# Optimization experiments

Hardware: AMD Instinct MI355X
Metric: run time of the kernel (lower is better)

## Reference

```python
import jax, jax.numpy as jnp
import numpy as np

B, T, I, H = 512, 256, 256, 512


def _lstm(x, Wih, Whh, bih, bhh):
    # x: [B, T, I]; Wih: [4H, I]; Whh: [4H, H]; gate order i, f, g, o (torch)
    Bv = x.shape[0]
    Hv = Whh.shape[1]
    xg = jnp.einsum('bti,gi->btg', x, Wih) + bih + bhh  # [B, T, 4H] (input projections hoisted out of scan)
    xg = jnp.transpose(xg, (1, 0, 2))  # [T, B, 4H]
    h0 = jnp.zeros((Bv, Hv), x.dtype)
    c0 = jnp.zeros((Bv, Hv), x.dtype)

    def step(carry, gx):
        h, c = carry
        g = gx + h @ Whh.T  # [B, 4H]
        i, f, gg, o = jnp.split(g, 4, axis=-1)
        i = jax.nn.sigmoid(i)
        f = jax.nn.sigmoid(f)
        gg = jnp.tanh(gg)
        o = jax.nn.sigmoid(o)
        c = f * c + i * gg
        h = o * jnp.tanh(c)
        return (h, c), h

    _, hs = jax.lax.scan(step, (h0, c0), xg)  # hs: [T, B, H]
    return jnp.transpose(hs, (1, 0, 2))  # [B, T, H]


def _bn1d(x, gamma, beta, eps=1e-5):
    # torch BatchNorm1d on [N, C, L] in training mode: per-channel stats over (N, L), biased var
    m = jnp.mean(x, axis=(0, 2), keepdims=True)
    v = jnp.var(x, axis=(0, 2), keepdims=True)
    return (x - m) * jax.lax.rsqrt(v + eps) * gamma[None, :, None] + beta[None, :, None]


def setup_inputs() -> dict:
    key = jax.random.key(0)
    ks = jax.random.split(key, 14)
    s = 1.0 / np.sqrt(H)
    return {
        'x': jax.random.normal(ks[0], (B, T, I), jnp.float32),
        'Wih': jax.random.uniform(ks[1], (4 * H, I), jnp.float32, -s, s),
        'Whh': jax.random.uniform(ks[2], (4 * H, H), jnp.float32, -s, s),
        'bih': jax.random.uniform(ks[3], (4 * H,), jnp.float32, -s, s),
        'bhh': jax.random.uniform(ks[4], (4 * H,), jnp.float32, -s, s),
        'fc1_w': jax.random.uniform(ks[5], (32, H), jnp.float32, -s, s),
        'fc1_b': jax.random.uniform(ks[6], (32,), jnp.float32, -s, s),
        'fc2_w': jax.random.uniform(ks[7], (1, 32), jnp.float32, -0.17, 0.17),
        'fc2_b': jax.random.uniform(ks[8], (1,), jnp.float32, -0.17, 0.17),
        'bn1_g': jnp.ones((T,), jnp.float32),
        'bn1_b': jnp.zeros((T,), jnp.float32),
        'bn2_g': jnp.ones((T,), jnp.float32),
        'bn2_b': jnp.zeros((T,), jnp.float32),
    }


def reference(x, Wih, Whh, bih, bhh, fc1_w, fc1_b, fc2_w, fc2_b, bn1_g, bn1_b, bn2_g, bn2_b):
    lstm_out = _lstm(x, Wih, Whh, bih, bhh)  # [B, T, H]
    a = jnp.einsum('bth,oh->bto', lstm_out, fc1_w) + fc1_b  # [B, T, 32]
    a = jax.nn.leaky_relu(_bn1d(a, bn1_g, bn1_b), negative_slope=0.1)
    z = jnp.einsum('bto,po->btp', a, fc2_w) + fc2_b  # [B, T, 1]
    out = jax.nn.relu(_bn1d(z, bn2_g, bn2_b))
    return out
```

## Files before the change

kernel.cpp:

```cpp
#include <hip/hip_runtime.h>

#define BB 512
#define TT 256
#define II 256
#define HH 512

typedef __attribute__((ext_vector_type(8))) short bf16x8;
typedef __attribute__((ext_vector_type(4))) float f32x4;

__device__ __forceinline__ unsigned short f2bf(float f) {
  union { float f; unsigned u; } v; v.f = f;
  unsigned r = v.u + 0x7fffu + ((v.u >> 16) & 1u);
  return (unsigned short)(r >> 16);
}

#define OFF_CNT   0
#define OFF_HSWZ  4096
#define OFF_XSWZ  1052672ULL
#define OFF_HIST  68161536ULL
#define ZERO_WORDS 263168

__global__ void zero_k(unsigned* __restrict__ p, int n) {
  int i = blockIdx.x * blockDim.x + threadIdx.x;
  if (i < n) p[i] = 0u;
}

__global__ __launch_bounds__(256) void prep_x(const float* __restrict__ x,
                                              unsigned char* __restrict__ ws) {
  __shared__ unsigned short xs[16][264];
  const int t = blockIdx.x >> 5, rc = blockIdx.x & 31;
  const int tid = threadIdx.x;
  {
    const int r = tid >> 4, seg = tid & 15;
    const float* src = x + ((size_t)(rc * 16 + r) * TT + t) * II + seg * 16;
    const float4* s4 = (const float4*)src;
#pragma unroll
    for (int q = 0; q < 4; ++q) {
      float4 v = s4[q];
      xs[r][seg * 16 + q * 4 + 0] = f2bf(v.x);
      xs[r][seg * 16 + q * 4 + 1] = f2bf(v.y);
      xs[r][seg * 16 + q * 4 + 2] = f2bf(v.z);
      xs[r][seg * 16 + q * 4 + 3] = f2bf(v.w);
    }
  }
  __syncthreads();
  const int lane = tid & 63;
  const int row16 = lane & 15, koff = (lane >> 4) * 8;
#pragma unroll
  for (int kc = tid >> 6; kc < 8; kc += 4) {
    union { unsigned short h[8]; uint4 v; } pk;
#pragma unroll
    for (int j = 0; j < 8; ++j) pk.h[j] = xs[row16][kc * 32 + koff + j];
    *(uint4*)(ws + OFF_XSWZ + (size_t)(t * 8 + kc) * 32768u +
              ((size_t)rc * 64 + lane) * 16) = pk.v;
  }
}

__global__ __launch_bounds__(512, 2) void lstm_persist(
    const float* __restrict__ Wih, const float* __restrict__ Whh,
    const float* __restrict__ bih, const float* __restrict__ bhh,
    unsigned char* __restrict__ ws)
{
  const int gid = blockIdx.x;
  const int g = gid & 31;
  const int m = gid >> 5;
  const int tid = threadIdx.x;
  const int wv = tid >> 6, lane = tid & 63;
  const int nh = wv & 3, kh = wv >> 2;
  const int lq = lane >> 4, ln = lane & 15;

  int* flags_g = (int*)(ws + (size_t)g * 128);
  unsigned char* xswz  = ws + OFF_XSWZ;
  unsigned char* hswz0 = ws + OFF_HSWZ;
  unsigned char* hswz1 = ws + OFF_HSWZ + 524288;
  unsigned char* hist  = ws + OFF_HIST;

  __shared__ int step_flag;
  if (tid == 0) step_flag = 0;

  bf16x8 Wf[12][4];
#pragma unroll
  for (int kk = 0; kk < 12; ++kk) {
    const int kb = (kh * 12 + kk) * 32 + lq * 8;
#pragma unroll
    for (int ns = 0; ns < 4; ++ns) {
      const int gcol = nh * 512 + m * 64 + ns * 16 + ln;
      const float* s = (kb < 256) ? (Wih + (size_t)gcol * 256 + kb)
                                  : (Whh + (size_t)gcol * 512 + (kb - 256));
      bf16x8 w;
#pragma unroll
      for (int j = 0; j < 8; ++j) w[j] = (short)f2bf(s[j]);
      Wf[kk][ns] = w;
    }
  }

  const int urow = tid >> 5;
  const int ujl  = (tid & 31) * 2;
  float bia2[2][4];
#pragma unroll
  for (int cc = 0; cc < 2; ++cc)
#pragma unroll
    for (int nt = 0; nt < 4; ++nt) {
      int gcol = nt * 512 + m * 64 + ujl + cc;
      bia2[cc][nt] = bih[gcol] + bhh[gcol];
    }

  __shared__ float g_s[8704];
  __shared__ float h_s[1088];
  __shared__ unsigned long long hstage[2048];

  float c2[2] = {0.f, 0.f};
  const f32x4 zero4 = {0.f, 0.f, 0.f, 0.f};

#pragma unroll 1
  for (int t = 0; t < 256; ++t) {
    unsigned char* hrd = (t & 1) ? hswz1 : hswz0;
    unsigned char* hwr = (t & 1) ? hswz0 : hswz1;

    f32x4 acc[4] = {zero4, zero4, zero4, zero4};

    if (kh == 0) {
#pragma unroll
      for (int kc = 0; kc < 8; ++kc) {
        bf16x8 a = *(const bf16x8*)(xswz + (size_t)(t * 8 + kc) * 32768u +
                                    ((size_t)(g * 64 + lane)) * 16);
#pragma unroll
        for (int ns = 0; ns < 4; ++ns)
          acc[ns] = __builtin_amdgcn_mfma_f32_16x16x32_bf16(a, Wf[kc][ns], acc[ns], 0, 0, 0);
      }
    }

    if (t > 0) {
      if (wv == 4) {
        int iter = 0;
        for (;;) {
          int v = __hip_atomic_load(flags_g + (lane & 7), __ATOMIC_RELAXED,
                                    __HIP_MEMORY_SCOPE_AGENT);
          if (__all(v >= t)) break;
          if (++iter >= (1 << 17)) break;
          __builtin_amdgcn_s_sleep(1);
        }
        __hip_atomic_store(&step_flag, t, __ATOMIC_RELAXED,
                           __HIP_MEMORY_SCOPE_WORKGROUP);
      } else {
        int iter = 0;
        while (__hip_atomic_load(&step_flag, __ATOMIC_RELAXED,
                                 __HIP_MEMORY_SCOPE_WORKGROUP) < t
               && iter < (1 << 20)) {
          ++iter;
          __builtin_amdgcn_s_sleep(1);
        }
      }
      asm volatile("" ::: "memory");
    }

    {
#pragma unroll
      for (int i = 0; i < 2; ++i) {
        const int p = (tid >> 6) + i * 8;
        const unsigned long long* src = (const unsigned long long*)
            (hrd + (size_t)p * 32768u + (size_t)g * 1024u + (size_t)lane * 16u);
        unsigned long long q0 = __hip_atomic_load(src + 0, __ATOMIC_RELAXED,
                                                  __HIP_MEMORY_SCOPE_AGENT);
        unsigned long long q1 = __hip_atomic_load(src + 1, __ATOMIC_RELAXED,
                                                  __HIP_MEMORY_SCOPE_AGENT);
        hstage[tid * 2 + i * 1024] = q0;
        hstage[tid * 2 + i * 1024 + 1] = q1;
      }
    }
    __syncthreads();

    const unsigned char* hs = (const unsigned char*)hstage;
    if (kh == 0) {
#pragma unroll
      for (int p = 0; p < 4; ++p) {
        bf16x8 a = *(const bf16x8*)(hs + p * 1024 + lane * 16);
#pragma unroll
        for (int ns = 0; ns < 4; ++ns)
          acc[ns] = __builtin_amdgcn_mfma_f32_16x16x32_bf16(a, Wf[8 + p][ns], acc[ns], 0, 0, 0);
      }
    } else {
#pragma unroll
      for (int kk = 0; kk < 12; ++kk) {
        bf16x8 a = *(const bf16x8*)(hs + (4 + kk) * 1024 + lane * 16);
#pragma unroll
        for (int ns = 0; ns < 4; ++ns)
          acc[ns] = __builtin_amdgcn_mfma_f32_16x16x32_bf16(a, Wf[kk][ns], acc[ns], 0, 0, 0);
      }
    }
#pragma unroll
    for (int ns = 0; ns < 4; ++ns)
#pragma unroll
      for (int r = 0; r < 4; ++r)
        g_s[((kh * 16 + lq * 4 + r) * 4 + nh) * 68 + ns * 16 + ln] = acc[ns][r];
    __syncthreads();

    {
#pragma unroll
      for (int cc = 0; cc < 2; ++cc) {
        const int jl = ujl + cc;
        float gi = g_s[((0 * 16 + urow) * 4 + 0) * 68 + jl]
                 + g_s[((1 * 16 + urow) * 4 + 0) * 68 + jl] + bia2[cc][0];
        float gf = g_s[((0 * 16 + urow) * 4 + 1) * 68 + jl]
                 + g_s[((1 * 16 + urow) * 4 + 1) * 68 + jl] + bia2[cc][1];
        float gg = g_s[((0 * 16 + urow) * 4 + 2) * 68 + jl]
                 + g_s[((1 * 16 + urow) * 4 + 2) * 68 + jl] + bia2[cc][2];
        float go = g_s[((0 * 16 + urow) * 4 + 3) * 68 + jl]
                 + g_s[((1 * 16 + urow) * 4 + 3) * 68 + jl] + bia2[cc][3];
        float iv = 1.f / (1.f + __expf(-gi));
        float fv = 1.f / (1.f + __expf(-gf));
        float gv = 1.f - 2.f / (__expf(2.f * gg) + 1.f);
        float ov = 1.f / (1.f + __expf(-go));
        float cv = fv * c2[cc] + iv * gv;
        c2[cc] = cv;
        h_s[urow * 68 + jl] = ov * (1.f - 2.f / (__expf(2.f * cv) + 1.f));
      }
    }
    __syncthreads();

    if (tid < 128) {
      int cc = tid >> 6;
      int lp = tid & 63;
      union { unsigned short s[8]; uint4 v; } pk;
#pragma unroll
      for (int j = 0; j < 8; ++j)
        pk.s[j] = f2bf(h_s[(lp & 15) * 68 + cc * 32 + (lp >> 4) * 8 + j]);
      *(uint4*)(hwr + (size_t)(2 * m + cc) * 32768u + (size_t)g * 1024u +
                (size_t)lp * 16u) = pk.v;
    }
    __syncthreads();

    if (tid == 0)
      __hip_atomic_store(flags_g + m, t + 1, __ATOMIC_RELAXED,
                         __HIP_MEMORY_SCOPE_AGENT);

    if (tid < 128) {
      int row = tid >> 3, jl0 = (tid & 7) * 8;
      union { unsigned short s[8]; uint4 v; } hq;
#pragma unroll
      for (int j = 0; j < 8; ++j) hq.s[j] = f2bf(h_s[row * 68 + jl0 + j]);
      int b = g * 16 + row;
      *(uint4*)(hist + ((size_t)(b * 256 + t) * 512 + m * 64 + jl0) * 2) = hq.v;
    }
  }
}

__global__ __launch_bounds__(256) void e1_fc1(
    const float* __restrict__ fc1_w, const unsigned char* __restrict__ hist,
    float* __restrict__ a_out)
{
  const int tid = threadIdx.x, wv = tid >> 6, lane = tid & 63;
  const int lq = lane >> 4, ln = lane & 15;

  bf16x8 Bf[16][2];
#pragma unroll
  for (int kk = 0; kk < 16; ++kk) {
#pragma unroll
    for (int nt = 0; nt < 2; ++nt) {
      const float* s = fc1_w + (size_t)(nt * 16 + ln) * 512 + kk * 32 + lq * 8;
      bf16x8 w;
#pragma unroll
      for (int j = 0; j < 8; ++j) w[j] = (short)f2bf(s[j]);
      Bf[kk][nt] = w;
    }
  }

  const int rbase = blockIdx.x * 128 + wv * 32;
  const f32x4 zero4 = {0.f, 0.f, 0.f, 0.f};
  f32x4 acc[2][2] = {{zero4, zero4}, {zero4, zero4}};
#pragma unroll
  for (int kk = 0; kk < 16; ++kk) {
    bf16x8 a0 = *(const bf16x8*)(hist + ((size_t)(rbase + ln) * 512 + kk * 32 + lq * 8) * 2);
    bf16x8 a1 = *(const bf16x8*)(hist + ((size_t)(rbase + 16 + ln) * 512 + kk * 32 + lq * 8) * 2);
#pragma unroll
    for (int nt = 0; nt < 2; ++nt) {
      acc[0][nt] = __builtin_amdgcn_mfma_f32_16x16x32_bf16(a0, Bf[kk][nt], acc[0][nt], 0, 0, 0);
      acc[1][nt] = __builtin_amdgcn_mfma_f32_16x16x32_bf16(a1, Bf[kk][nt], acc[1][nt], 0, 0, 0);
    }
  }
#pragma unroll
  for (int mt = 0; mt < 2; ++mt)
#pragma unroll
    for (int nt = 0; nt < 2; ++nt)
#pragma unroll
      for (int r = 0; r < 4; ++r) {
        int row = rbase + mt * 16 + lq * 4 + r;
        a_out[(size_t)row * 32 + nt * 16 + ln] = acc[mt][nt][r];
      }
}

__global__ __launch_bounds__(256) void e2_head(
    const float* __restrict__ a_in, const float* __restrict__ fc1_b,
    const float* __restrict__ fc2_w, const float* __restrict__ fc2_b,
    const float* __restrict__ bn1_g, const float* __restrict__ bn1_b,
    const float* __restrict__ bn2_g, const float* __restrict__ bn2_b,
    float* __restrict__ out)
{
  const int t = blockIdx.x, tid = threadIdx.x;
  __shared__ float fb[32], fw[32];
  __shared__ float red[4][2], red2[4][2];
  if (tid < 32) { fb[tid] = fc1_b[tid]; fw[tid] = fc2_w[tid]; }
  __syncthreads();

  float va[2][32];
  float s1 = 0.f, s2 = 0.f;
#pragma unroll
  for (int rr = 0; rr < 2; ++rr) {
    int b = tid * 2 + rr;
    const float* p = a_in + ((size_t)b * 256 + t) * 32;
#pragma unroll
    for (int o = 0; o < 32; ++o) {
      float v = p[o] + fb[o];
      va[rr][o] = v;
      s1 += v; s2 += v * v;
    }
  }
#pragma unroll
  for (int off = 32; off > 0; off >>= 1) {
    s1 += __shfl_down(s1, off);
    s2 += __shfl_down(s2, off);
  }
  if ((tid & 63) == 0) { red[tid >> 6][0] = s1; red[tid >> 6][1] = s2; }
  __syncthreads();
  float tot1 = red[0][0] + red[1][0] + red[2][0] + red[3][0];
  float tot2 = red[0][1] + red[1][1] + red[2][1] + red[3][1];
  float m1 = tot1 * (1.f / 16384.f);
  float v1 = tot2 * (1.f / 16384.f) - m1 * m1;
  float sc1 = bn1_g[t] * rsqrtf(v1 + 1e-5f);
  float sh1 = bn1_b[t];

  float z[2];
  float zs1 = 0.f, zs2 = 0.f;
#pragma unroll
  for (int rr = 0; rr < 2; ++rr) {
    float acc = fc2_b[0];
#pragma unroll
    for (int o = 0; o < 32; ++o) {
      float av = (va[rr][o] - m1) * sc1 + sh1;
      av = (av > 0.f) ? av : 0.1f * av;
      acc += av * fw[o];
    }
    z[rr] = acc; zs1 += acc; zs2 += acc * acc;
  }
#pragma unroll
  for (int off = 32; off > 0; off >>= 1) {
    zs1 += __shfl_down(zs1, off);
    zs2 += __shfl_down(zs2, off);
  }
  if ((tid & 63) == 0) { red2[tid >> 6][0] = zs1; red2[tid >> 6][1] = zs2; }
  __syncthreads();
  float zt1 = red2[0][0] + red2[1][0] + red2[2][0] + red2[3][0];
  float zt2 = red2[0][1] + red2[1][1] + red2[2][1] + red2[3][1];
  float m2 = zt1 * (1.f / 512.f);
  float v2 = zt2 * (1.f / 512.f) - m2 * m2;
  float sc2 = bn2_g[t] * rsqrtf(v2 + 1e-5f);
  float sh2 = bn2_b[t];
#pragma unroll
  for (int rr = 0; rr < 2; ++rr) {
    int b = tid * 2 + rr;
    float res = (z[rr] - m2) * sc2 + sh2;
    out[(size_t)b * 256 + t] = (res > 0.f) ? res : 0.f;
  }
}

extern "C" void kernel_launch(void* const* d_in, const int* in_sizes, int n_in,
                              void* d_out, int out_size, void* d_ws, size_t ws_size,
                              hipStream_t stream) {
  const float* x    = (const float*)d_in[0];
  const float* Wih  = (const float*)d_in[1];
  const float* Whh  = (const float*)d_in[2];
  const float* bih  = (const float*)d_in[3];
  const float* bhh  = (const float*)d_in[4];
  const float* fc1w = (const float*)d_in[5];
  const float* fc1b = (const float*)d_in[6];
  const float* fc2w = (const float*)d_in[7];
  const float* fc2b = (const float*)d_in[8];
  const float* b1g  = (const float*)d_in[9];
  const float* b1b  = (const float*)d_in[10];
  const float* b2g  = (const float*)d_in[11];
  const float* b2b  = (const float*)d_in[12];
  unsigned char* ws = (unsigned char*)d_ws;
  float* out = (float*)d_out;
  float* a_buf = (float*)(ws + OFF_XSWZ);

  zero_k<<<1028, 256, 0, stream>>>((unsigned*)ws, ZERO_WORDS);
  prep_x<<<8192, 256, 0, stream>>>(x, ws);
  lstm_persist<<<256, 512, 0, stream>>>(Wih, Whh, bih, bhh, ws);
  e1_fc1<<<1024, 256, 0, stream>>>(fc1w, ws + OFF_HIST, a_buf);
  e2_head<<<256, 256, 0, stream>>>(a_buf, fc1b, fc2w, fc2b, b1g, b1b, b2g, b2b, out);
}
```

Measured before the change: 1.484 ms.

## Replace block-wide flag wait and LDS h staging with per-wave partial polling

```diff
diff --git a/kernel.cpp b/kernel.cpp
--- a/kernel.cpp
+++ b/kernel.cpp
@@ -12,6 +12,16 @@
   union { float f; unsigned u; } v; v.f = f;
   unsigned r = v.u + 0x7fffu + ((v.u >> 16) & 1u);
   return (unsigned short)(r >> 16);
+}
+
+__device__ __forceinline__ void pollw(const int* p, int t) {
+  int iter = 0;
+  for (;;) {
+    int v = __hip_atomic_load(p, __ATOMIC_RELAXED, __HIP_MEMORY_SCOPE_AGENT);
+    if (__all(v >= t)) break;
+    if (++iter >= (1 << 17)) break;
+    __builtin_amdgcn_s_sleep(1);
+  }
 }
 
 #define OFF_CNT   0
@@ -75,8 +85,10 @@
   unsigned char* hswz1 = ws + OFF_HSWZ + 524288;
   unsigned char* hist  = ws + OFF_HIST;
 
-  __shared__ int step_flag;
-  if (tid == 0) step_flag = 0;
+  const int lr3 = lane % 3;
+  const int* p01  = flags_g + (lane & 1);
+  const int* p234 = flags_g + 2 + lr3;
+  const int* p567 = flags_g + 5 + lr3;
 
   bf16x8 Wf[12][4];
 #pragma unroll
@@ -107,7 +119,6 @@
 
   __shared__ float g_s[8704];
   __shared__ float h_s[1088];
-  __shared__ unsigned long long hstage[2048];
 
   float c2[2] = {0.f, 0.f};
   const f32x4 zero4 = {0.f, 0.f, 0.f, 0.f};
@@ -118,6 +129,7 @@
     unsigned char* hwr = (t & 1) ? hswz0 : hswz1;
 
     f32x4 acc[4] = {zero4, zero4, zero4, zero4};
+    const unsigned char* hbase = hrd + (size_t)g * 1024u + (size_t)lane * 16u;
 
     if (kh == 0) {
 #pragma unroll
@@ -128,64 +140,48 @@
         for (int ns = 0; ns < 4; ++ns)
           acc[ns] = __builtin_amdgcn_mfma_f32_16x16x32_bf16(a, Wf[kc][ns], acc[ns], 0, 0, 0);
       }
-    }
-
-    if (t > 0) {
-      if (wv == 4) {
-        int iter = 0;
-        for (;;) {
-          int v = __hip_atomic_load(flags_g + (lane & 7), __ATOMIC_RELAXED,
-                                    __HIP_MEMORY_SCOPE_AGENT);
-          if (__all(v >= t)) break;
-          if (++iter >= (1 << 17)) break;
-          __builtin_amdgcn_s_sleep(1);
+      if (t > 0) { pollw(p01, t); asm volatile("" ::: "memory"); }
+      unsigned long long u0[4], u1[4];
+#pragma unroll
+      for (int p = 0; p < 4; ++p) {
+        const unsigned long long* q =
+            (const unsigned long long*)(hbase + (size_t)p * 32768u);
+        u0[p] = __hip_atomic_load(q + 0, __ATOMIC_RELAXED, __HIP_MEMORY_SCOPE_AGENT);
+        u1[p] = __hip_atomic_load(q + 1, __ATOMIC_RELAXED, __HIP_MEMORY_SCOPE_AGENT);
+      }
+#pragma unroll
+      for (int kk = 0; kk < 4; ++kk) {
+        union { unsigned long long q[2]; bf16x8 v; } u;
+        u.q[0] = u0[kk]; u.q[1] = u1[kk];
+#pragma unroll
+        for (int ns = 0; ns < 4; ++ns)
+          acc[ns] = __builtin_amdgcn_mfma_f32_16x16x32_bf16(u.v, Wf[8 + kk][ns], acc[ns], 0, 0, 0);
+      }
+    } else {
+      if (t > 0) { pollw(p234, t); asm volatile("" ::: "memory"); }
+      unsigned long long u0[6], u1[6];
+#pragma unroll
+      for (int p = 0; p < 6; ++p) {
+        const unsigned long long* q =
+            (const unsigned long long*)(hbase + (size_t)(4 + p) * 32768u);
+        u0[p] = __hip_atomic_load(q + 0, __ATOMIC_RELAXED, __HIP_MEMORY_SCOPE_AGENT);
+        u1[p] = __hip_atomic_load(q + 1, __ATOMIC_RELAXED, __HIP_MEMORY_SCOPE_AGENT);
+      }
+      if (t > 0) { pollw(p567, t); asm volatile("" ::: "memory"); }
+#pragma unroll
+      for (int kk = 0; kk < 12; ++kk) {
+        const int slot = kk % 6;
+        union { unsigned long long q[2]; bf16x8 v; } u;
+        u.q[0] = u0[slot]; u.q[1] = u1[slot];
+        if (kk < 6) {
+          const unsigned long long* q =
+              (const unsigned long long*)(hbase + (size_t)(10 + kk) * 32768u);
+          u0[slot] = __hip_atomic_load(q + 0, __ATOMIC_RELAXED, __HIP_MEMORY_SCOPE_AGENT);
+          u1[slot] = __hip_atomic_load(q + 1, __ATOMIC_RELAXED, __HIP_MEMORY_SCOPE_AGENT);
         }
-        __hip_atomic_store(&step_flag, t, __ATOMIC_RELAXED,
-                           __HIP_MEMORY_SCOPE_WORKGROUP);
-      } else {
-        int iter = 0;
-        while (__hip_atomic_load(&step_flag, __ATOMIC_RELAXED,
-                                 __HIP_MEMORY_SCOPE_WORKGROUP) < t
-               && iter < (1 << 20)) {
-          ++iter;
-          __builtin_amdgcn_s_sleep(1);
-        }
-      }
-      asm volatile("" ::: "memory");
-    }
-
-    {
-#pragma unroll
-      for (int i = 0; i < 2; ++i) {
-        const int p = (tid >> 6) + i * 8;
-        const unsigned long long* src = (const unsigned long long*)
-            (hrd + (size_t)p * 32768u + (size_t)g * 1024u + (size_t)lane * 16u);
-        unsigned long long q0 = __hip_atomic_load(src + 0, __ATOMIC_RELAXED,
-                                                  __HIP_MEMORY_SCOPE_AGENT);
-        unsigned long long q1 = __hip_atomic_load(src + 1, __ATOMIC_RELAXED,
-                                                  __HIP_MEMORY_SCOPE_AGENT);
-        hstage[tid * 2 + i * 1024] = q0;
-        hstage[tid * 2 + i * 1024 + 1] = q1;
-      }
-    }
-    __syncthreads();
-
-    const unsigned char* hs = (const unsigned char*)hstage;
-    if (kh == 0) {
-#pragma unroll
-      for (int p = 0; p < 4; ++p) {
-        bf16x8 a = *(const bf16x8*)(hs + p * 1024 + lane * 16);
 #pragma unroll
         for (int ns = 0; ns < 4; ++ns)
-          acc[ns] = __builtin_amdgcn_mfma_f32_16x16x32_bf16(a, Wf[8 + p][ns], acc[ns], 0, 0, 0);
-      }
-    } else {
-#pragma unroll
-      for (int kk = 0; kk < 12; ++kk) {
-        bf16x8 a = *(const bf16x8*)(hs + (4 + kk) * 1024 + lane * 16);
-#pragma unroll
-        for (int ns = 0; ns < 4; ++ns)
-          acc[ns] = __builtin_amdgcn_mfma_f32_16x16x32_bf16(a, Wf[kk][ns], acc[ns], 0, 0, 0);
+          acc[ns] = __builtin_amdgcn_mfma_f32_16x16x32_bf16(u.v, Wf[kk][ns], acc[ns], 0, 0, 0);
       }
     }
 #pragma unroll
```

Result: faster. 1.412 ms (-4.8%).
